# Kernel tuning notes

Hardware: AMD Instinct MI355X
Metric: run time of the kernel (lower is better)

Reference implementation:

```python
import jax, jax.numpy as jnp
import numpy as np

PAD = 4  # init_kwargs pad


def setup_inputs() -> dict:
    key = jax.random.key(0)
    k1, k2 = jax.random.split(key)
    x = jax.random.normal(k1, (1024, 4, 84, 84), dtype=jnp.float32)
    shift = jax.random.randint(k2, (1024, 1, 1, 2), 0, 2 * PAD + 1, dtype=jnp.int32)
    return {"x": x, "shift": shift}


def _random_shift_aug(x, shift, pad):
    n, c, h, w = x.shape
    # replicate pad on H and W (matches F.pad(..., 'replicate'))
    xp = jnp.pad(x, ((0, 0), (0, 0), (pad, pad), (pad, pad)), mode='edge')
    Hp, Wp = h + 2 * pad, w + 2 * pad

    # base grid: normalized centers of the first w/h pixels of the padded image
    eps_x = 1.0 / Wp
    ax = jnp.linspace(-1.0 + eps_x, 1.0 - eps_x, Wp, dtype=x.dtype)[:w]  # (w,)
    eps_y = 1.0 / (h + 2 * 4)  # NOTE: original code hardcodes 4 here, not pad
    ay = jnp.linspace(-1.0 + eps_y, 1.0 - eps_y, h + 2 * 4, dtype=x.dtype)[:h]  # (h,)

    scale = jnp.asarray(2.0 / (h + 2 * pad), dtype=x.dtype)
    sx = shift[..., 0].astype(x.dtype) * scale  # (n,1,1)
    sy = shift[..., 1].astype(x.dtype) * scale  # (n,1,1)

    gx = ax[None, None, :] + sx  # (n,1,w) normalized x coords
    gy = ay[None, :, None] + sy  # (n,h,1) normalized y coords

    # grid_sample unnormalization, align_corners=False
    ix = ((gx + 1.0) * Wp - 1.0) * 0.5  # (n,1,w)
    iy = ((gy + 1.0) * Hp - 1.0) * 0.5  # (n,h,1)

    ix0f = jnp.floor(ix)
    iy0f = jnp.floor(iy)
    wx = (ix - ix0f)[..., None]  # (n,1,w,1)
    wy = (iy - iy0f)[..., None]  # (n,h,1,1)
    ix0 = ix0f.astype(jnp.int32)
    iy0 = iy0f.astype(jnp.int32)

    b = jnp.arange(n, dtype=jnp.int32)[:, None, None]  # (n,1,1)

    def corner(iyi, ixi):
        # zeros padding_mode: mask out-of-bounds taps
        valid = ((ixi >= 0) & (ixi < Wp) & (iyi >= 0) & (iyi < Hp)).astype(x.dtype)
        v = xp[b, :, jnp.clip(iyi, 0, Hp - 1), jnp.clip(ixi, 0, Wp - 1)]  # (n,h,w,c)
        return v * valid[..., None]

    v00 = corner(iy0, ix0)
    v01 = corner(iy0, ix0 + 1)
    v10 = corner(iy0 + 1, ix0)
    v11 = corner(iy0 + 1, ix0 + 1)

    out = (v00 * (1 - wy) * (1 - wx) + v01 * (1 - wy) * wx
           + v10 * wy * (1 - wx) + v11 * wy * wx)  # (n,h,w,c)
    return jnp.transpose(out, (0, 3, 1, 2))  # (n,c,h,w)


def reference(x, shift):
    return _random_shift_aug(x, shift, PAD)
```

## Files before the change

kernel.cpp:

```cpp
#include <hip/hip_runtime.h>


#define HW 84
#define PADV 4
#define PLANE (HW * HW)
#define PF4   (PLANE / 4)
#define NTHR  256
#define K     7

struct __attribute__((aligned(4))) f4u { float x, y, z, w; };

__device__ __forceinline__ float pick(const f4u& v, int idx) {
    return (idx < 1) ? v.x : (idx < 2) ? v.y : (idx < 3) ? v.z : v.w;
}

__global__ __launch_bounds__(NTHR)
void shift_aug_kernel(const float* __restrict__ x,
                      const int* __restrict__ shift,
                      float* __restrict__ out) {
    const int tid = threadIdx.x;
    const int b   = blockIdx.x;
    const int n   = b >> 2;

    const int sx = shift[2 * n]     - PADV;
    const int sy = shift[2 * n + 1] - PADV;

    const float* __restrict__ plane  = x   + (size_t)b * PLANE;
    float*       __restrict__ oplane = out + (size_t)b * PLANE;

    f4u L[K];
    #pragma unroll
    for (int i = 0; i < K; ++i) {
        const int g   = tid + NTHR * i;
        const int gi  = (g < PF4) ? g : (PF4 - 1);
        const int row = gi / 21;
        const int tx  = gi - row * 21;
        const int srow = min(max(row + sy, 0), HW - 1);
        const int cb   = 4 * tx + sx;
        const int B    = min(max(cb, 0), HW - 4);
        L[i] = *(const f4u*)(plane + srow * HW + B);
    }

    __builtin_amdgcn_sched_barrier(0);

    #pragma unroll
    for (int i = 0; i < K; ++i) {
        const int g   = tid + NTHR * i;
        const int gi  = (g < PF4) ? g : (PF4 - 1);
        const int row = gi / 21;
        const int tx  = gi - row * 21;
        const int cb  = 4 * tx + sx;
        const int B   = min(max(cb, 0), HW - 4);
        const int d   = cb - B;

        float4 o;
        o.x = pick(L[i], min(max(d,     0), 3));
        o.y = pick(L[i], min(max(d + 1, 0), 3));
        o.z = pick(L[i], min(max(d + 2, 0), 3));
        o.w = pick(L[i], min(max(d + 3, 0), 3));

        if (i < K - 1) {
            ((float4*)oplane)[g] = o;
        } else if (g < PF4) {
            ((float4*)oplane)[g] = o;
        }
    }
}

extern "C" void kernel_launch(void* const* d_in, const int* in_sizes, int n_in,
                              void* d_out, int out_size, void* d_ws, size_t ws_size,
                              hipStream_t stream) {
    const float* x     = (const float*)d_in[0];
    const int*   shift = (const int*)d_in[1];
    float*       out   = (float*)d_out;

    dim3 block(NTHR, 1, 1);
    dim3 grid(4096, 1, 1);
    shift_aug_kernel<<<grid, block, 0, stream>>>(x, shift, out);
}
```

Measured before the change: 203.4 us.

## Process whole image per block with software-pipelined single-load loop

Each block now handles all 4 channels of one image (1024 blocks instead of 4096) and iterates 28 times. A rolled loop prefetches the next float4 while it stores the current one, replacing the 7 loads issued up front. The goal is to cut block launch overhead and the tail waste from the partial last iteration. In exchange each thread keeps only one load in flight instead of seven, and there are fewer blocks to hide memory latency.

```diff
diff --git a/kernel.cpp b/kernel.cpp
--- a/kernel.cpp
+++ b/kernel.cpp
@@ -1,17 +1,32 @@
 #include <hip/hip_runtime.h>
 
 
-#define HW 84
-#define PADV 4
+#define HW    84
+#define PADV  4
 #define PLANE (HW * HW)
-#define PF4   (PLANE / 4)
+#define QPP   (PLANE / 4)
+#define QPI   (4 * QPP)
 #define NTHR  256
-#define K     7
+#define NIT   28
 
+typedef float f32x4 __attribute__((ext_vector_type(4)));
 struct __attribute__((aligned(4))) f4u { float x, y, z, w; };
 
 __device__ __forceinline__ float pick(const f4u& v, int idx) {
     return (idx < 1) ? v.x : (idx < 2) ? v.y : (idx < 3) ? v.z : v.w;
+}
+
+__device__ __forceinline__ int src_addr(int G, int sx, int sy, int& d) {
+    G = min(G, QPI - 1);
+    const int c    = G / QPP;
+    const int gi   = G - c * QPP;
+    const int row  = gi / 21;
+    const int tx   = gi - row * 21;
+    const int srow = min(max(row + sy, 0), HW - 1);
+    const int cb   = 4 * tx + sx;
+    const int B    = min(max(cb, 0), HW - 4);
+    d = cb - B;
+    return c * PLANE + srow * HW + B;
 }
 
 __global__ __launch_bounds__(NTHR)
@@ -19,51 +34,41 @@
                       const int* __restrict__ shift,
                       float* __restrict__ out) {
     const int tid = threadIdx.x;
-    const int b   = blockIdx.x;
-    const int n   = b >> 2;
+    const int n   = blockIdx.x;
 
     const int sx = shift[2 * n]     - PADV;
     const int sy = shift[2 * n + 1] - PADV;
 
-    const float* __restrict__ plane  = x   + (size_t)b * PLANE;
-    float*       __restrict__ oplane = out + (size_t)b * PLANE;
+    const float* __restrict__ img  = x   + (size_t)n * (4 * PLANE);
+    float*       __restrict__ oimg = out + (size_t)n * (4 * PLANE);
 
-    f4u L[K];
-    #pragma unroll
-    for (int i = 0; i < K; ++i) {
-        const int g   = tid + NTHR * i;
-        const int gi  = (g < PF4) ? g : (PF4 - 1);
-        const int row = gi / 21;
-        const int tx  = gi - row * 21;
-        const int srow = min(max(row + sy, 0), HW - 1);
-        const int cb   = 4 * tx + sx;
-        const int B    = min(max(cb, 0), HW - 4);
-        L[i] = *(const f4u*)(plane + srow * HW + B);
+    int dcur;
+    f4u L = *(const f4u*)(img + src_addr(tid, sx, sy, dcur));
+
+    #pragma unroll 1
+    for (int j = 0; j < NIT - 1; ++j) {
+        int dnext;
+        const f4u Ln = *(const f4u*)(img + src_addr(tid + NTHR * (j + 1), sx, sy, dnext));
+
+        float4 o;
+        o.x = pick(L, min(max(dcur,     0), 3));
+        o.y = pick(L, min(max(dcur + 1, 0), 3));
+        o.z = pick(L, min(max(dcur + 2, 0), 3));
+        o.w = pick(L, min(max(dcur + 3, 0), 3));
+        ((float4*)oimg)[tid + NTHR * j] = o;
+
+        L = Ln;
+        dcur = dnext;
     }
 
-    __builtin_amdgcn_sched_barrier(0);
-
-    #pragma unroll
-    for (int i = 0; i < K; ++i) {
-        const int g   = tid + NTHR * i;
-        const int gi  = (g < PF4) ? g : (PF4 - 1);
-        const int row = gi / 21;
-        const int tx  = gi - row * 21;
-        const int cb  = 4 * tx + sx;
-        const int B   = min(max(cb, 0), HW - 4);
-        const int d   = cb - B;
-
+    {
         float4 o;
-        o.x = pick(L[i], min(max(d,     0), 3));
-        o.y = pick(L[i], min(max(d + 1, 0), 3));
-        o.z = pick(L[i], min(max(d + 2, 0), 3));
-        o.w = pick(L[i], min(max(d + 3, 0), 3));
-
-        if (i < K - 1) {
-            ((float4*)oplane)[g] = o;
-        } else if (g < PF4) {
-            ((float4*)oplane)[g] = o;
-        }
+        o.x = pick(L, min(max(dcur,     0), 3));
+        o.y = pick(L, min(max(dcur + 1, 0), 3));
+        o.z = pick(L, min(max(dcur + 2, 0), 3));
+        o.w = pick(L, min(max(dcur + 3, 0), 3));
+        const int G = tid + NTHR * (NIT - 1);
+        if (G < QPI) ((float4*)oimg)[G] = o;
     }
 }
 
@@ -75,6 +80,6 @@
     float*       out   = (float*)d_out;
 
     dim3 block(NTHR, 1, 1);
-    dim3 grid(4096, 1, 1);
+    dim3 grid(1024, 1, 1);
     shift_aug_kernel<<<grid, block, 0, stream>>>(x, shift, out);
 }
```

After: 208.8 us. 2.6% more time.
